# Performance work log

Measured on AMD Instinct MI355X. Metric: run time of the kernel, lower is better.

Reference implementation:

```python
import jax, jax.numpy as jnp
import numpy as np

B, C, H, W = 16, 256, 56, 56
HEADS = 4
C_OUT = 256
K = 3
SQ = 16  # squeeze_rate (C=256 >= 80, so not halved)
BN_EPS = 1e-5


def setup_inputs() -> dict:
    key = jax.random.key(0)
    ks = jax.random.split(key, 9)
    r = C // SQ
    cper = C_OUT // HEADS
    return {
        "x": jax.random.normal(ks[0], (B, C, H, W), dtype=jnp.float32),
        "bn_gamma": 1.0 + 0.1 * jax.random.normal(ks[1], (C,), dtype=jnp.float32),
        "bn_beta": 0.1 * jax.random.normal(ks[2], (C,), dtype=jnp.float32),
        "bn_mean": 0.1 * jax.random.normal(ks[3], (C,), dtype=jnp.float32),
        "bn_var": 0.5 + jax.random.uniform(ks[4], (C,), dtype=jnp.float32),
        "fc1_w": 0.1 * jax.random.normal(ks[5], (HEADS, r, C), dtype=jnp.float32),
        "fc2_w": 0.1 * jax.random.normal(ks[6], (HEADS, C, r), dtype=jnp.float32),
        "fc2_b": jnp.ones((HEADS, C), dtype=jnp.float32),  # init.constant_(bias, 1.0)
        "conv_w": 0.05 * jax.random.normal(ks[7], (HEADS, cper, C, K, K), dtype=jnp.float32),
        "inactive_channels": 192,
    }


def reference(x, bn_gamma, bn_beta, bn_mean, bn_var, fc1_w, fc2_w, fc2_b, conv_w, inactive_channels):
    b, c, h, w = x.shape
    heads = fc1_w.shape[0]
    # BatchNorm (inference, running stats) + ReLU
    inv = jax.lax.rsqrt(bn_var + BN_EPS)
    xn = jax.nn.relu((x - bn_mean[None, :, None, None]) * (bn_gamma * inv)[None, :, None, None]
                     + bn_beta[None, :, None, None])
    # Global average pool -> [b, c]
    x_avg = xn.mean(axis=(2, 3))
    # Per-head SE gate: relu(fc2(relu(fc1(x_avg))))  -> [heads, b, c]
    y1 = jax.nn.relu(jnp.einsum("bc,hrc->hbr", x_avg, fc1_w))
    mask = jax.nn.relu(jnp.einsum("hbr,hcr->hbc", y1, fc2_w) + fc2_b[:, None, :])
    lasso_loss = mask.mean(axis=(1, 2)).sum()  # sum over heads of per-head mean
    # topk smallest -> threshold; zero out mask values <= k-th smallest (detached cmp)
    mask_d = jax.lax.stop_gradient(mask)
    if inactive_channels > 0:
        neg_vals, _ = jax.lax.top_k(-mask_d, inactive_channels)  # k largest of -mask
        thresh = -neg_vals[..., -1:]  # k-th smallest of mask, [heads, b, 1]
        mask_c = jnp.where(mask_d <= thresh, 0.0, mask)
    else:
        mask_c = mask
    # Apply per-head channel mask and stack heads: [b, heads*c, h, w]
    mc = jnp.transpose(mask_c, (1, 0, 2))  # [b, heads, c]
    x_mask = (xn[:, None, :, :, :] * mc[:, :, :, None, None]).reshape(b, heads * c, h, w)
    # Grouped conv (groups=heads), weight [heads*cper, c, K, K]
    wflat = conv_w.reshape(-1, c, K, K)
    out = jax.lax.conv_general_dilated(
        x_mask, wflat, window_strides=(1, 1), padding=[(1, 1), (1, 1)],
        dimension_numbers=("NCHW", "OIHW", "NCHW"), feature_group_count=heads)
    bo, co, ho, wo = out.shape
    out = out.reshape(bo, heads, co // heads, ho, wo).transpose(0, 2, 1, 3, 4).reshape(bo, co, ho, wo)
    return out, lasso_loss
```

## Files before the change

### kernel.cpp

```cpp
#include <hip/hip_runtime.h>
#include <hip/hip_bf16.h>
#include <math.h>

#define B_     16
#define C_     256
#define H_     56
#define W_     56
#define HEADS_ 4
#define CPER_  64
#define R_     16
#define HW_    (H_*W_)
#define BN_EPS_ 1e-5f

typedef short bf16x8 __attribute__((ext_vector_type(8)));
typedef float f32x4  __attribute__((ext_vector_type(4)));

__device__ inline unsigned short f2bf(float f) {
    unsigned int u = __builtin_bit_cast(unsigned int, f);
    u += 0x7fffu + ((u >> 16) & 1u);
    return (unsigned short)(u >> 16);
}

__global__ __launch_bounds__(256) void k_pool(
    const float* __restrict__ x,
    const float* __restrict__ gamma, const float* __restrict__ beta,
    const float* __restrict__ mean,  const float* __restrict__ var,
    float* __restrict__ xavg)
{
    int wv = threadIdx.x >> 6, ln = threadIdx.x & 63;
    int plane = blockIdx.x * 4 + wv;
    int c = plane & (C_ - 1);
    float s = gamma[c] * rsqrtf(var[c] + BN_EPS_);
    float t = fmaf(-mean[c], s, beta[c]);
    const float4* xp = (const float4*)(x + (size_t)plane * HW_);
    float sum = 0.f;
    for (int i = ln; i < HW_ / 4; i += 64) {
        float4 v = xp[i];
        sum += fmaxf(fmaf(v.x, s, t), 0.f) + fmaxf(fmaf(v.y, s, t), 0.f)
             + fmaxf(fmaf(v.z, s, t), 0.f) + fmaxf(fmaf(v.w, s, t), 0.f);
    }
    for (int off = 32; off; off >>= 1) sum += __shfl_down(sum, off, 64);
    if (ln == 0) xavg[plane] = sum * (1.f / HW_);
}

__global__ __launch_bounds__(256) void k_se_wg(
    const float* __restrict__ xavg,
    const float* __restrict__ fc1, const float* __restrict__ fc2,
    const float* __restrict__ fc2b, const int* __restrict__ kptr,
    const float* __restrict__ convw,
    int* __restrict__ aidx64, float* __restrict__ lasso,
    short* __restrict__ Wc)
{
    int hb = blockIdx.x;
    int h = hb / B_, b = hb - h * B_;
    int tid = threadIdx.x;

    __shared__ float sav[C_], sy1[R_], smask[C_], sred[4], sthr;
    __shared__ int scnt, s_ord[C_];
    __shared__ int s_act[64];
    __shared__ float s_mv[64];
    __shared__ short sO[9 * 4096];

    sav[tid] = xavg[b * C_ + tid];
    if (tid == 0) scnt = 0;
    __syncthreads();

    if (tid < R_) {
        const float* w = fc1 + (size_t)(h * R_ + tid) * C_;
        float acc = 0.f;
        for (int c2 = 0; c2 < C_; ++c2) acc = fmaf(sav[c2], w[c2], acc);
        sy1[tid] = fmaxf(acc, 0.f);
    }
    __syncthreads();

    const float* w2 = fc2 + (size_t)(h * C_ + tid) * R_;
    float acc = fc2b[h * C_ + tid];
    for (int r = 0; r < R_; ++r) acc = fmaf(sy1[r], w2[r], acc);
    float m = fmaxf(acc, 0.f);
    smask[tid] = m;
    __syncthreads();

    float ls = m;
    for (int off = 32; off > 0; off >>= 1) ls += __shfl_down(ls, off, 64);
    int lane = tid & 63, wv = tid >> 6;
    if (lane == 0) sred[wv] = ls;

    int cl = 0, ce = 0;
    for (int j = 0; j < C_; ++j) {
        float vj = smask[j];
        cl += (vj < m);
        ce += (vj == m);
    }
    if (tid == 0) sthr = -1e30f;
    __syncthreads();
    int k = kptr[0];
    if (k > 0 && cl <= k - 1 && (k - 1) < cl + ce) sthr = m;
    __syncthreads();

    float thr = sthr;
    float mc = (m <= thr) ? 0.f : m;
    if (mc != 0.f) {
        int p = atomicAdd(&scnt, 1);
        s_ord[p] = tid;
    }
    __syncthreads();
    if (tid < 64) {
        int a = (tid < scnt) ? s_ord[tid] : 0;
        aidx64[hb * 64 + tid] = a;
        s_act[tid] = a;
        s_mv[tid]  = (tid < scnt) ? smask[a] : 0.f;
    }
    if (tid == 0)
        atomicAdd(lasso, (sred[0] + sred[1] + sred[2] + sred[3]) * (1.f / (B_ * C_)));
    __syncthreads();

    const float* wsrc = convw + (size_t)h * CPER_ * C_ * 9;
    for (int it = 0; it < 16; ++it) {
        int e = it * 256 + tid;
        int cp = e & 63, j = e >> 6;
        const float* wp = wsrc + ((size_t)j * C_ + s_act[cp]) * 9;
        float mv = s_mv[cp];
        int slot = (cp + 8 * (j & 7)) & 63;
        #pragma unroll
        for (int t = 0; t < 9; ++t)
            sO[t * 4096 + j * 64 + slot] = (short)f2bf(wp[t] * mv);
    }
    __syncthreads();
    short* wdst = Wc + (size_t)hb * 9 * 4096;
    for (int it = 0; it < 18; ++it) {
        int e = it * 256 + tid;
        *(bf16x8*)&wdst[e * 8] = *(const bf16x8*)&sO[e * 8];
    }
}

__global__ __launch_bounds__(256) void k_bnc(
    const float* __restrict__ x,
    const float* __restrict__ gamma, const float* __restrict__ beta,
    const float* __restrict__ mean,  const float* __restrict__ var,
    const int* __restrict__ aidx64, short* __restrict__ xc)
{
    int y = blockIdx.x, b = blockIdx.y;
    int tid = threadIdx.x;
    int h = tid >> 6;
    __shared__ __align__(16) unsigned short T[W_ * 256];

    int c = aidx64[(h * B_ + b) * 64 + (tid & 63)];
    float s = gamma[c] * rsqrtf(var[c] + BN_EPS_);
    float t0 = fmaf(-mean[c], s, beta[c]);
    const float* xrow = x + ((size_t)(b * C_ + c)) * HW_ + y * W_;
    #pragma unroll
    for (int f = 0; f < 14; ++f) {
        float4 v = *(const float4*)(xrow + f * 4);
        int px = f * 4;
        T[(px + 0) * 256 + tid] = f2bf(fmaxf(fmaf(v.x, s, t0), 0.f));
        T[(px + 1) * 256 + tid] = f2bf(fmaxf(fmaf(v.y, s, t0), 0.f));
        T[(px + 2) * 256 + tid] = f2bf(fmaxf(fmaf(v.z, s, t0), 0.f));
        T[(px + 3) * 256 + tid] = f2bf(fmaxf(fmaf(v.w, s, t0), 0.f));
    }
    __syncthreads();

    const uint2* Ts = (const uint2*)T;
    uint2* ob = (uint2*)xc;
    #pragma unroll
    for (int it = 0; it < 14; ++it) {
        int e = it * 256 + tid;
        int px = e >> 6, col4 = e & 63;
        int hh = col4 >> 4, cp4 = col4 & 15;
        uint2 v = Ts[px * 64 + col4];
        ob[((size_t)(hh * B_ + b) * HW_ + (size_t)y * W_ + px) * 16 + cp4] = v;
    }
}

__global__ __launch_bounds__(512, 2) void k_conv(
    const short* __restrict__ xc, const short* __restrict__ Wc,
    float* __restrict__ out)
{
    int g = blockIdx.x;
    int vx = g & 7, r = g >> 3;
    int hb = vx * 8 + r / 14;
    int sub = r - (r / 14) * 14;
    int band = sub >> 1, xh = sub & 1;
    int h = hb >> 4, b = hb & 15;
    int tid = threadIdx.x, lane = tid & 63, wv = tid >> 6;
    int m = lane & 15, q = lane >> 4;
    int yrow = band * 8 + wv;
    int xbase = xh * 32;
    int arot = q * 8 + 8 * (m & 7);

    __shared__ short sW[9 * 4096];

    const short* Wh = Wc + (size_t)hb * 9 * 4096;
    const short* xb = xc + (size_t)hb * HW_ * 64 + q * 8;

    bf16x8 bFb[4][2];
    bf16x8 aFb[2][4];

#define LOADB_(kk) { \
        const int t_ = (kk) >> 1, c0_ = ((kk) & 1) * 32; \
        const int dy_ = t_ / 3 - 1, dx_ = t_ % 3 - 1; \
        int gy_ = yrow + dy_; \
        bool ok_ = (unsigned)gy_ < (unsigned)H_; \
        _Pragma("unroll") \
        for (int xt_ = 0; xt_ < 2; ++xt_) { \
            int gx_ = xbase + xt_ * 16 + m + dx_; \
            bf16x8 v_ = {0, 0, 0, 0, 0, 0, 0, 0}; \
            if (ok_ && (unsigned)gx_ < (unsigned)W_) \
                v_ = *(const bf16x8*)(xb + ((size_t)(gy_ * W_ + gx_)) * 64 + c0_); \
            bFb[(kk) & 3][xt_] = v_; \
        } }

#define LOADA_(kk) { \
        const int t_ = (kk) >> 1, c0_ = ((kk) & 1) * 32; \
        const short* sWc_ = sW + t_ * 4096; \
        _Pragma("unroll") \
        for (int jt_ = 0; jt_ < 4; ++jt_) \
            aFb[(kk) & 1][jt_] = *(const bf16x8*)&sWc_[(jt_ * 16 + m) * 64 + ((c0_ + arot) & 63)]; \
        }

    LOADB_(0);
    LOADB_(1);
    LOADB_(2);

    #pragma unroll
    for (int it = 0; it < 9; ++it) {
        int e = it * 512 + tid;
        *(bf16x8*)&sW[e * 8] = *(const bf16x8*)(Wh + e * 8);
    }
    __syncthreads();

    f32x4 acc[4][2];
    #pragma unroll
    for (int i = 0; i < 4; ++i)
        #pragma unroll
        for (int j = 0; j < 2; ++j)
            #pragma unroll
            for (int rr = 0; rr < 4; ++rr) acc[i][j][rr] = 0.f;

    LOADA_(0);

    #pragma unroll
    for (int k = 0; k < 18; ++k) {
        if (k + 3 < 18) LOADB_(k + 3);
        if (k + 1 < 18) LOADA_(k + 1);
        #pragma unroll
        for (int jt = 0; jt < 4; ++jt)
            #pragma unroll
            for (int xt = 0; xt < 2; ++xt)
                acc[jt][xt] = __builtin_amdgcn_mfma_f32_16x16x32_bf16(
                    aFb[k & 1][jt], bFb[k & 3][xt], acc[jt][xt], 0, 0, 0);
    }
#undef LOADB_
#undef LOADA_

    #pragma unroll
    for (int xt = 0; xt < 2; ++xt) {
        int xx = xbase + xt * 16 + m;
        if (xx < W_) {
            #pragma unroll
            for (int jt = 0; jt < 4; ++jt)
                #pragma unroll
                for (int rr = 0; rr < 4; ++rr) {
                    int j = jt * 16 + q * 4 + rr;
                    int oc = j * HEADS_ + h;
                    out[(((size_t)b * C_ + oc) * H_ + yrow) * W_ + xx] = acc[jt][xt][rr];
                }
        }
    }
}

extern "C" void kernel_launch(void* const* d_in, const int* in_sizes, int n_in,
                              void* d_out, int out_size, void* d_ws, size_t ws_size,
                              hipStream_t stream)
{
    const float* x     = (const float*)d_in[0];
    const float* gamma = (const float*)d_in[1];
    const float* beta  = (const float*)d_in[2];
    const float* mean  = (const float*)d_in[3];
    const float* var   = (const float*)d_in[4];
    const float* fc1   = (const float*)d_in[5];
    const float* fc2   = (const float*)d_in[6];
    const float* fc2b  = (const float*)d_in[7];
    const float* convw = (const float*)d_in[8];
    const int*   kptr  = (const int*)d_in[9];

    float* out   = (float*)d_out;
    float* lasso = out + (size_t)B_ * C_ * HW_;

    char* ws = (char*)d_ws;
    size_t off = 0;
    short* xc    = (short*)(ws + off); off += (size_t)HEADS_ * B_ * HW_ * 64 * 2;
    off = (off + 255) & ~(size_t)255;
    float* xavg  = (float*)(ws + off); off += (size_t)B_ * C_ * 4;
    int*   aidx64= (int*)  (ws + off); off += (size_t)HEADS_ * B_ * 64 * 4;
    off = (off + 255) & ~(size_t)255;
    short* Wc    = (short*)(ws + off); off += (size_t)HEADS_ * B_ * 9 * CPER_ * 64 * 2;

    hipMemsetAsync(lasso, 0, 4, stream);

    k_pool<<<B_ * C_ / 4, 256, 0, stream>>>(x, gamma, beta, mean, var, xavg);
    k_se_wg<<<HEADS_ * B_, 256, 0, stream>>>(xavg, fc1, fc2, fc2b, kptr, convw,
                                             aidx64, lasso, Wc);
    k_bnc<<<dim3(H_, B_), 256, 0, stream>>>(x, gamma, beta, mean, var, aidx64, xc);
    k_conv<<<HEADS_ * B_ * 14, 512, 0, stream>>>(xc, Wc, out);
}
```

Measured before the change: 193.6 us.

## Split SE weight-gather across blocks, unroll pool loads, split conv into two launches

The pool kernel is unrolled with four independent accumulators and explicit float4 loads, which raises memory-level parallelism. The SE and weight-prep kernel now runs on a 2D grid in which each of four blocks per head-batch builds a 16-output-channel slice of the masked weights. This cuts the shared memory per block and spreads the work across more blocks, at the cost of recomputing the SE gate four times. Compaction of the active channels now uses wave ballots and popcounts instead of a shared atomic counter. The result is deterministic ordering instead of atomic-dependent ordering, which also makes aidx64 consistent across the redundant blocks. The conv kernel is launched twice, each launch covering half of the head-batch pairs, which adds launch overhead and may change scheduling or tail behavior.

```diff
diff --git a/kernel.cpp b/kernel.cpp
--- a/kernel.cpp
+++ b/kernel.cpp
@@ -33,12 +33,28 @@
     float s = gamma[c] * rsqrtf(var[c] + BN_EPS_);
     float t = fmaf(-mean[c], s, beta[c]);
     const float4* xp = (const float4*)(x + (size_t)plane * HW_);
-    float sum = 0.f;
-    for (int i = ln; i < HW_ / 4; i += 64) {
-        float4 v = xp[i];
-        sum += fmaxf(fmaf(v.x, s, t), 0.f) + fmaxf(fmaf(v.y, s, t), 0.f)
-             + fmaxf(fmaf(v.z, s, t), 0.f) + fmaxf(fmaf(v.w, s, t), 0.f);
-    }
+    float s0 = 0.f, s1 = 0.f, s2 = 0.f, s3 = 0.f;
+    #pragma unroll
+    for (int i = 0; i < 3; ++i) {
+        float4 a = xp[ln + (i * 4 + 0) * 64];
+        float4 b2 = xp[ln + (i * 4 + 1) * 64];
+        float4 c2 = xp[ln + (i * 4 + 2) * 64];
+        float4 d = xp[ln + (i * 4 + 3) * 64];
+        s0 += fmaxf(fmaf(a.x, s, t), 0.f) + fmaxf(fmaf(a.y, s, t), 0.f)
+            + fmaxf(fmaf(a.z, s, t), 0.f) + fmaxf(fmaf(a.w, s, t), 0.f);
+        s1 += fmaxf(fmaf(b2.x, s, t), 0.f) + fmaxf(fmaf(b2.y, s, t), 0.f)
+            + fmaxf(fmaf(b2.z, s, t), 0.f) + fmaxf(fmaf(b2.w, s, t), 0.f);
+        s2 += fmaxf(fmaf(c2.x, s, t), 0.f) + fmaxf(fmaf(c2.y, s, t), 0.f)
+            + fmaxf(fmaf(c2.z, s, t), 0.f) + fmaxf(fmaf(c2.w, s, t), 0.f);
+        s3 += fmaxf(fmaf(d.x, s, t), 0.f) + fmaxf(fmaf(d.y, s, t), 0.f)
+            + fmaxf(fmaf(d.z, s, t), 0.f) + fmaxf(fmaf(d.w, s, t), 0.f);
+    }
+    if (ln < 16) {
+        float4 e = xp[768 + ln];
+        s0 += fmaxf(fmaf(e.x, s, t), 0.f) + fmaxf(fmaf(e.y, s, t), 0.f)
+            + fmaxf(fmaf(e.z, s, t), 0.f) + fmaxf(fmaf(e.w, s, t), 0.f);
+    }
+    float sum = (s0 + s1) + (s2 + s3);
     for (int off = 32; off; off >>= 1) sum += __shfl_down(sum, off, 64);
     if (ln == 0) xavg[plane] = sum * (1.f / HW_);
 }
@@ -52,17 +68,18 @@
     short* __restrict__ Wc)
 {
     int hb = blockIdx.x;
+    int j0 = blockIdx.y * 16;
     int h = hb / B_, b = hb - h * B_;
     int tid = threadIdx.x;
 
     __shared__ float sav[C_], sy1[R_], smask[C_], sred[4], sthr;
-    __shared__ int scnt, s_ord[C_];
+    __shared__ int s_ord[C_];
+    __shared__ unsigned long long sbal[4];
     __shared__ int s_act[64];
     __shared__ float s_mv[64];
-    __shared__ short sO[9 * 4096];
+    __shared__ short sO[9 * 1024];
 
     sav[tid] = xavg[b * C_ + tid];
-    if (tid == 0) scnt = 0;
     __syncthreads();
 
     if (tid < R_) {
@@ -80,9 +97,9 @@
     smask[tid] = m;
     __syncthreads();
 
+    int lane = tid & 63, wv = tid >> 6;
     float ls = m;
     for (int off = 32; off > 0; off >>= 1) ls += __shfl_down(ls, off, 64);
-    int lane = tid & 63, wv = tid >> 6;
     if (lane == 0) sred[wv] = ls;
 
     int cl = 0, ce = 0;
@@ -99,37 +116,52 @@
 
     float thr = sthr;
     float mc = (m <= thr) ? 0.f : m;
-    if (mc != 0.f) {
-        int p = atomicAdd(&scnt, 1);
-        s_ord[p] = tid;
-    }
-    __syncthreads();
+
+    bool active = (mc != 0.f);
+    unsigned long long bal = __ballot(active);
+    if (lane == 0) sbal[wv] = bal;
+    __syncthreads();
+    int base = 0, total = 0;
+    #pragma unroll
+    for (int w = 0; w < 4; ++w) {
+        int pc = __popcll(sbal[w]);
+        if (w < wv) base += pc;
+        total += pc;
+    }
+    if (active)
+        s_ord[base + __popcll(bal & ((1ull << lane) - 1ull))] = tid;
+    __syncthreads();
+
     if (tid < 64) {
-        int a = (tid < scnt) ? s_ord[tid] : 0;
-        aidx64[hb * 64 + tid] = a;
+        int a = (tid < total) ? s_ord[tid] : 0;
         s_act[tid] = a;
-        s_mv[tid]  = (tid < scnt) ? smask[a] : 0.f;
-    }
-    if (tid == 0)
+        s_mv[tid]  = (tid < total) ? smask[a] : 0.f;
+        if (blockIdx.y == 0) aidx64[hb * 64 + tid] = a;
+    }
+    if (tid == 0 && blockIdx.y == 0)
         atomicAdd(lasso, (sred[0] + sred[1] + sred[2] + sred[3]) * (1.f / (B_ * C_)));
     __syncthreads();
 
     const float* wsrc = convw + (size_t)h * CPER_ * C_ * 9;
-    for (int it = 0; it < 16; ++it) {
+    for (int it = 0; it < 4; ++it) {
         int e = it * 256 + tid;
-        int cp = e & 63, j = e >> 6;
+        int cp = e & 63, jj = e >> 6;
+        int j = j0 + jj;
         const float* wp = wsrc + ((size_t)j * C_ + s_act[cp]) * 9;
         float mv = s_mv[cp];
         int slot = (cp + 8 * (j & 7)) & 63;
         #pragma unroll
         for (int t = 0; t < 9; ++t)
-            sO[t * 4096 + j * 64 + slot] = (short)f2bf(wp[t] * mv);
-    }
-    __syncthreads();
-    short* wdst = Wc + (size_t)hb * 9 * 4096;
-    for (int it = 0; it < 18; ++it) {
-        int e = it * 256 + tid;
-        *(bf16x8*)&wdst[e * 8] = *(const bf16x8*)&sO[e * 8];
+            sO[t * 1024 + jj * 64 + slot] = (short)f2bf(wp[t] * mv);
+    }
+    __syncthreads();
+    short* wdst = Wc + (size_t)hb * 9 * 4096 + j0 * 64;
+    for (int it = 0; it < 5; ++it) {
+        int v = it * 256 + tid;
+        if (v < 1152) {
+            int t = v >> 7, r8 = v & 127;
+            *(bf16x8*)&wdst[t * 4096 + r8 * 8] = *(const bf16x8*)&sO[t * 1024 + r8 * 8];
+        }
     }
 }
 
@@ -173,12 +205,13 @@
 
 __global__ __launch_bounds__(512, 2) void k_conv(
     const short* __restrict__ xc, const short* __restrict__ Wc,
-    float* __restrict__ out)
+    float* __restrict__ out, int hbhalf)
 {
     int g = blockIdx.x;
     int vx = g & 7, r = g >> 3;
-    int hb = vx * 8 + r / 14;
-    int sub = r - (r / 14) * 14;
+    int b14 = r / 14;
+    int sub = r - b14 * 14;
+    int hb = vx * 8 + hbhalf * 4 + b14;
     int band = sub >> 1, xh = sub & 1;
     int h = hb >> 4, b = hb & 15;
     int tid = threadIdx.x, lane = tid & 63, wv = tid >> 6;
@@ -298,8 +331,9 @@
     hipMemsetAsync(lasso, 0, 4, stream);
 
     k_pool<<<B_ * C_ / 4, 256, 0, stream>>>(x, gamma, beta, mean, var, xavg);
-    k_se_wg<<<HEADS_ * B_, 256, 0, stream>>>(xavg, fc1, fc2, fc2b, kptr, convw,
-                                             aidx64, lasso, Wc);
+    k_se_wg<<<dim3(HEADS_ * B_, 4), 256, 0, stream>>>(xavg, fc1, fc2, fc2b, kptr, convw,
+                                                      aidx64, lasso, Wc);
     k_bnc<<<dim3(H_, B_), 256, 0, stream>>>(x, gamma, beta, mean, var, aidx64, xc);
-    k_conv<<<HEADS_ * B_ * 14, 512, 0, stream>>>(xc, Wc, out);
-}
+    k_conv<<<448, 512, 0, stream>>>(xc, Wc, out, 0);
+    k_conv<<<448, 512, 0, stream>>>(xc, Wc, out, 1);
+}
```

After: 187.0 us. 3.4% less time.
